# Performance work log

Hardware: AMD Instinct MI355X
Metric: run time of the kernel (lower is better)

Reference implementation:

```python
import jax, jax.numpy as jnp
import numpy as np

L, E, H, D, F, B, CIN, N = 12, 128, 4, 32, 512, 64, 256, 257


def setup_inputs() -> dict:
    key = jax.random.key(0)
    ks = jax.random.split(key, 10)
    s = 0.02
    rn = lambda k, shape: jax.random.normal(k, shape, jnp.float32) * s
    return {
        "feat": jax.random.normal(ks[0], (B, CIN, 32, 32), jnp.float32),
        "conv_w": rn(ks[1], (E, CIN, 3, 3)),
        "conv_b": jnp.zeros((E,), jnp.float32),
        "pos_emb": rn(ks[2], (1, N, E)),
        "cls_token": rn(ks[3], (1, 1, E)),
        "ln1_s": jnp.ones((L, E), jnp.float32),
        "ln1_b": jnp.zeros((L, E), jnp.float32),
        "qkv_w": rn(ks[4], (L, 3 * E, E)),
        "qkv_b": jnp.zeros((L, 3 * E), jnp.float32),
        "proj_w": rn(ks[5], (L, E, E)),
        "proj_b": jnp.zeros((L, E), jnp.float32),
        "ln2_s": jnp.ones((L, E), jnp.float32),
        "ln2_b": jnp.zeros((L, E), jnp.float32),
        "ffn1_w": rn(ks[6], (L, F, E)),
        "ffn1_b": jnp.zeros((L, F), jnp.float32),
        "ffn2_w": rn(ks[7], (L, E, F)),
        "ffn2_b": jnp.zeros((L, E), jnp.float32),
        "fn_s": jnp.ones((E,), jnp.float32),
        "fn_b": jnp.zeros((E,), jnp.float32),
        "fc_w": rn(ks[8], (2, E)),
        "fc_b": jnp.zeros((2,), jnp.float32),
    }


def _ln(x, s, b, eps):
    m = jnp.mean(x, -1, keepdims=True)
    v = jnp.mean((x - m) ** 2, -1, keepdims=True)
    return (x - m) * jax.lax.rsqrt(v + eps) * s + b


def reference(feat, conv_w, conv_b, pos_emb, cls_token, ln1_s, ln1_b, qkv_w,
              qkv_b, proj_w, proj_b, ln2_s, ln2_b, ffn1_w, ffn1_b, ffn2_w,
              ffn2_b, fn_s, fn_b, fc_w, fc_b):
    # patch embed: 3x3 conv stride 2 -> 16x16 = 256 tokens
    emb = jax.lax.conv_general_dilated(
        feat, conv_w, (2, 2), ((1, 1), (1, 1)),
        dimension_numbers=("NCHW", "OIHW", "NCHW")) + conv_b[None, :, None, None]
    Bsz = emb.shape[0]
    emb = emb.reshape(Bsz, E, -1).transpose(0, 2, 1)  # [B, 256, E]
    x = jnp.concatenate([jnp.broadcast_to(cls_token, (Bsz, 1, E)), emb], axis=1)
    x = x + pos_emb  # [B, N, E]
    scale = (E // H) ** -0.5

    def block(x, p):
        l1s, l1b, qw, qb, pw, pb, l2s, l2b, w1, b1, w2, b2 = p
        h = _ln(x, l1s, l1b, 1e-5)
        qkv = (h @ qw.T + qb).reshape(Bsz, N, 3, H, D).transpose(2, 0, 3, 1, 4)
        q, k, v = qkv[0], qkv[1], qkv[2]  # [B, H, N, D]
        att = jax.nn.softmax(jnp.einsum("bhnd,bhmd->bhnm", q, k) * scale, axis=-1)
        o = jnp.einsum("bhnm,bhmd->bhnd", att, v).transpose(0, 2, 1, 3).reshape(Bsz, N, E)
        x = x + (o @ pw.T + pb)
        h2 = _ln(x, l2s, l2b, 1e-5)
        x = x + (jax.nn.gelu(h2 @ w1.T + b1, approximate=False) @ w2.T + b2)
        return x, None

    x, _ = jax.lax.scan(block, x, (ln1_s, ln1_b, qkv_w, qkv_b, proj_w, proj_b,
                                   ln2_s, ln2_b, ffn1_w, ffn1_b, ffn2_w, ffn2_b))
    x = _ln(x, fn_s, fn_b, 1e-6)
    out_feat = x[:, 0, :]
    out = out_feat @ fc_w.T + fc_b
    return (out, out_feat)
```

## Files before the change

### kernel.cpp

```cpp
#include <hip/hip_runtime.h>
#include <math.h>

constexpr int NP_ = 272;
constexpr int MP_ = 64 * NP_;
constexpr int TPB_ = 17;

typedef short short8 __attribute__((ext_vector_type(8)));
typedef float f32x4 __attribute__((ext_vector_type(4)));

__device__ inline short f2bs(float f) {
    unsigned u = __builtin_bit_cast(unsigned, f);
    unsigned r = (u + 0x7fffu + ((u >> 16) & 1u)) >> 16;
    return (short)r;
}

__device__ inline f32x4 mfma16(short8 a, short8 b, f32x4 c) {
    return __builtin_amdgcn_mfma_f32_16x16x32_bf16(a, b, c, 0, 0, 0);
}

__global__ void repack_all(const float* __restrict__ qkvw, const float* __restrict__ projw,
                           const float* __restrict__ f1w, const float* __restrict__ f2w,
                           const float* __restrict__ convw,
                           short* __restrict__ wq, short* __restrict__ wp,
                           short* __restrict__ w1, short* __restrict__ w2,
                           short* __restrict__ wc) {
    int o = blockIdx.x * 256 + threadIdx.x;
    if (o < 589824) {
        int l = o / 49152, r = o % 49152;
        int chunk = r / 3072, w = r % 3072;
        int n = w >> 3, k = chunk * 8 + (w & 7);
        wq[o] = f2bs(qkvw[(size_t)l * 49152 + n * 128 + k]);
        return;
    }
    o -= 589824;
    if (o < 196608) {
        int l = o / 16384, r = o % 16384;
        int chunk = r / 1024, w = r % 1024;
        int n = w >> 3, k = chunk * 8 + (w & 7);
        wp[o] = f2bs(projw[(size_t)l * 16384 + n * 128 + k]);
        return;
    }
    o -= 196608;
    if (o < 786432) {
        int l = o / 65536, r = o % 65536;
        int chunk = r / 4096, w = r % 4096;
        int n = w >> 3, k = chunk * 8 + (w & 7);
        w1[o] = f2bs(f1w[(size_t)l * 65536 + n * 128 + k]);
        return;
    }
    o -= 786432;
    if (o < 786432) {
        int l = o / 65536, r = o % 65536;
        int chunk = r / 1024, w = r % 1024;
        int n = w >> 3, k = chunk * 8 + (w & 7);
        w2[o] = f2bs(f2w[(size_t)l * 65536 + n * 512 + k]);
        return;
    }
    o -= 786432;
    if (o < 294912) {
        int j = o & 7;
        int col = (o >> 3) & 127;
        int c = o >> 10;
        int qd = c & 3, cscb = c >> 2;
        int cs = cscb & 7, kykx = cscb >> 3;
        int cin = cs * 32 + qd * 8 + j;
        int ky = kykx / 3, kx = kykx % 3;
        wc[o] = f2bs(convw[((col * 256 + cin) * 3 + ky) * 3 + kx]);
    }
}

__global__ __launch_bounds__(256) void conv_gemm(const float* __restrict__ feat, const short* __restrict__ wr,
                                                 const float* __restrict__ cb, const float* __restrict__ pos,
                                                 const float* __restrict__ cls, float* __restrict__ X) {
    __shared__ __align__(16) short Ain[3 * 34 * 256];
    int b = blockIdx.x >> 4, oy = blockIdx.x & 15;
    int tid = threadIdx.x;
    for (int idx = tid; idx < 6144; idx += 256) {
        int x4 = idx & 7;
        int cin = (idx >> 3) & 255;
        int r = idx >> 11;
        int y = 2 * oy + r - 1;
        float4 f = make_float4(0.f, 0.f, 0.f, 0.f);
        if (y >= 0 && y < 32)
            f = *(const float4*)(feat + (((size_t)(b * 256 + cin) * 32 + y) * 32 + x4 * 4));
        int cg = cin >> 3, c7 = cin & 7;
        float vv[4] = {f.x, f.y, f.z, f.w};
#pragma unroll
        for (int dx = 0; dx < 4; ++dx) {
            int px = x4 * 4 + 1 + dx;
            int sw = (px >> 1) & 7;
            Ain[(r * 34 + px) * 256 + ((cg ^ sw) * 8) + c7] = f2bs(vv[dx]);
        }
    }
    for (int idx = tid; idx < 1536; idx += 256) {
        int c = idx & 255;
        int j = idx >> 8;
        int r = j >> 1;
        int px = (j & 1) ? 33 : 0;
        Ain[(r * 34 + px) * 256 + c] = 0;
    }
    __syncthreads();
    int wave = tid >> 6, lane = tid & 63;
    int ng = wave, lo = lane & 15, qd = lane >> 4;
    f32x4 acc[2] = {};
#pragma unroll
    for (int ky = 0; ky < 3; ++ky)
#pragma unroll
        for (int kx = 0; kx < 3; ++kx) {
            int sx = 2 * lo + kx;
            int arow = (ky * 34 + sx) * 256;
            int sw = (sx >> 1) & 7;
            const short* wb = wr + (((size_t)((ky * 3 + kx) * 8) * 4 + qd) * 128 + ng * 32 + lo) * 8;
#pragma unroll
            for (int cs = 0; cs < 8; ++cs) {
                short8 af = *(const short8*)(Ain + arow + (((cs * 4 + qd) ^ sw) * 8));
                short8 b0 = *(const short8*)(wb + (size_t)cs * 4096);
                short8 b1 = *(const short8*)(wb + (size_t)cs * 4096 + 128);
                acc[0] = mfma16(af, b0, acc[0]);
                acc[1] = mfma16(af, b1, acc[1]);
            }
        }
#pragma unroll
    for (int t = 0; t < 2; ++t) {
        int e = ng * 32 + t * 16 + lo;
        float bias = cb[e];
#pragma unroll
        for (int r = 0; r < 4; ++r) {
            int tok = 1 + oy * 16 + qd * 4 + r;
            X[((size_t)b * NP_ + tok) * 128 + e] = acc[t][r] + bias + pos[tok * 128 + e];
        }
    }
    if (oy == 0) {
        if (tid < 128) X[(size_t)b * NP_ * 128 + tid] = cls[tid] + pos[tid];
        for (int idx = tid; idx < 15 * 128; idx += 256)
            X[((size_t)b * NP_ + 257) * 128 + idx] = 0.f;
    }
}

__device__ inline void ln_tile16(const float* Xl, const float* __restrict__ s, const float* __restrict__ bb,
                                 short* SB, int tid, float eps) {
    int wv = tid >> 6, lane = tid & 63;
    int r4 = lane & 3, c32 = lane >> 2;
    int row = wv * 4 + r4;
    const float* xr = Xl + row * 132 + c32 * 8;
    float4 a = *(const float4*)(xr);
    float4 b = *(const float4*)(xr + 4);
    float v[8] = {a.x, a.y, a.z, a.w, b.x, b.y, b.z, b.w};
    float sum = v[0] + v[1] + v[2] + v[3] + v[4] + v[5] + v[6] + v[7];
    sum += __shfl_xor(sum, 4); sum += __shfl_xor(sum, 8);
    sum += __shfl_xor(sum, 16); sum += __shfl_xor(sum, 32);
    float mean = sum * (1.f / 128.f);
    float vs = 0.f;
#pragma unroll
    for (int j = 0; j < 8; ++j) { float d = v[j] - mean; vs += d * d; }
    vs += __shfl_xor(vs, 4); vs += __shfl_xor(vs, 8);
    vs += __shfl_xor(vs, 16); vs += __shfl_xor(vs, 32);
    float rs = rsqrtf(vs * (1.f / 128.f) + eps);
    float4 s0 = *(const float4*)(s + c32 * 8), s1 = *(const float4*)(s + c32 * 8 + 4);
    float4 b0 = *(const float4*)(bb + c32 * 8), b1 = *(const float4*)(bb + c32 * 8 + 4);
    float sv[8] = {s0.x, s0.y, s0.z, s0.w, s1.x, s1.y, s1.z, s1.w};
    float bv[8] = {b0.x, b0.y, b0.z, b0.w, b1.x, b1.y, b1.z, b1.w};
    short8 o;
#pragma unroll
    for (int j = 0; j < 8; ++j) o[j] = f2bs((v[j] - mean) * rs * sv[j] + bv[j]);
    *(short8*)(SB + (c32 * 16 + row) * 8) = o;
}

__device__ inline void qkv_stage32(const short* SB, const short* __restrict__ wq, const float* __restrict__ qb,
                                   const short8* pre, int mg, int wv, int lo, int qd,
                                   short* __restrict__ Qf, short* __restrict__ Kf, short* __restrict__ Vt) {
    int n0 = wv * 96;
    f32x4 acc[2][6] = {};
#pragma unroll
    for (int ki = 0; ki < 4; ++ki) {
        int kq = ki * 4 + qd;
        short8 a0 = *(const short8*)(SB + (kq * 16 + lo) * 8);
        short8 a1 = *(const short8*)(SB + 2048 + (kq * 16 + lo) * 8);
#pragma unroll
        for (int t = 0; t < 6; ++t) {
            short8 bf = (ki == 0) ? pre[t]
                                  : *(const short8*)(wq + ((size_t)kq * 384 + n0 + t * 16 + lo) * 8);
            acc[0][t] = mfma16(a0, bf, acc[0][t]);
            acc[1][t] = mfma16(a1, bf, acc[1][t]);
        }
    }
#pragma unroll
    for (int mt = 0; mt < 2; ++mt)
#pragma unroll
        for (int t = 0; t < 6; ++t) {
            int n = n0 + t * 16 + lo;
            float bvv = qb[n];
            int seg = n >> 7, m = n & 127, h = m >> 5, d = m & 31;
#pragma unroll
            for (int r = 0; r < 4; ++r) {
                int row = mg * 32 + mt * 16 + qd * 4 + r;
                int bb2 = row / NP_, q = row - bb2 * NP_;
                short val = f2bs(acc[mt][t][r] + bvv);
                if (seg == 2)
                    Vt[((size_t)(bb2 * 4 + h) * 32 + d) * NP_ + q] = val;
                else
                    (seg ? Kf : Qf)[((size_t)(bb2 * 4 + h) * 4 + (d >> 3)) * (NP_ * 8) + q * 8 + (d & 7)] = val;
            }
        }
}

__global__ __launch_bounds__(256, 3) void qkv0(const float* __restrict__ X, const short* __restrict__ wq,
                                               const float* __restrict__ qb, const float* __restrict__ ls,
                                               const float* __restrict__ lb,
                                               short* __restrict__ Qf, short* __restrict__ Kf,
                                               short* __restrict__ Vt) {
    __shared__ __align__(16) float Xl[32 * 132];
    __shared__ __align__(16) short SB[2 * 2048];
    int mg = blockIdx.x, tid = threadIdx.x;
    int wv = tid >> 6, lane = tid & 63, lo = lane & 15, qd = lane >> 4;
    for (int idx = tid; idx < 1024; idx += 256) {
        int tok = idx >> 5, c = idx & 31;
        *(float4*)(Xl + tok * 132 + c * 4) = *(const float4*)(X + (size_t)(mg * 32 + tok) * 128 + c * 4);
    }
    short8 preq[6];
#pragma unroll
    for (int t = 0; t < 6; ++t)
        preq[t] = *(const short8*)(wq + ((size_t)qd * 384 + wv * 96 + t * 16 + lo) * 8);
    __syncthreads();
    ln_tile16(Xl, ls, lb, SB, tid, 1e-5f);
    ln_tile16(Xl + 16 * 132, ls, lb, SB + 2048, tid, 1e-5f);
    __syncthreads();
    qkv_stage32(SB, wq, qb, preq, mg, wv, lo, qd, Qf, Kf, Vt);
}

template <int LAST>
__global__ __launch_bounds__(256, 3) void layer_tail(
    const short* __restrict__ Of, const short* __restrict__ wp, const float* __restrict__ pb,
    const float* __restrict__ l2s, const float* __restrict__ l2b,
    const short* __restrict__ w1, const float* __restrict__ b1,
    const short* __restrict__ w2, const float* __restrict__ b2,
    float* __restrict__ X,
    const float* __restrict__ l1s, const float* __restrict__ l1b,
    const short* __restrict__ wq, const float* __restrict__ qb,
    short* __restrict__ Qf, short* __restrict__ Kf, short* __restrict__ Vt) {
    __shared__ __align__(16) short SB[2 * 2048];
    __shared__ __align__(16) float Xl[32 * 132];
    __shared__ __align__(16) short Uh[2 * 32 * 136];
    int mg = blockIdx.x, tid = threadIdx.x;
    int wv = tid >> 6, lane = tid & 63, lo = lane & 15, qd = lane >> 4;
    const short* osrc = Of + (size_t)mg * 4096;
    for (int idx = tid; idx < 512; idx += 256)
        *(short8*)(SB + idx * 8) = *(const short8*)(osrc + idx * 8);
    for (int idx = tid; idx < 1024; idx += 256) {
        int tok = idx >> 5, c = idx & 31;
        *(float4*)(Xl + tok * 132 + c * 4) = *(const float4*)(X + (size_t)(mg * 32 + tok) * 128 + c * 4);
    }
    int n0 = wv * 32;
    short8 prep[8];
#pragma unroll
    for (int ki = 0; ki < 4; ++ki) {
        int kq = ki * 4 + qd;
        prep[ki * 2] = *(const short8*)(wp + ((size_t)kq * 128 + n0 + lo) * 8);
        prep[ki * 2 + 1] = *(const short8*)(wp + ((size_t)kq * 128 + n0 + 16 + lo) * 8);
    }
    __syncthreads();
    {
        f32x4 pa[2][2] = {};
#pragma unroll
        for (int ki = 0; ki < 4; ++ki) {
            int kq = ki * 4 + qd;
            short8 a0 = *(const short8*)(SB + (kq * 16 + lo) * 8);
            short8 a1 = *(const short8*)(SB + 2048 + (kq * 16 + lo) * 8);
            pa[0][0] = mfma16(a0, prep[ki * 2], pa[0][0]);
            pa[0][1] = mfma16(a0, prep[ki * 2 + 1], pa[0][1]);
            pa[1][0] = mfma16(a1, prep[ki * 2], pa[1][0]);
            pa[1][1] = mfma16(a1, prep[ki * 2 + 1], pa[1][1]);
        }
        float pb0 = pb[n0 + lo], pb1 = pb[n0 + 16 + lo];
#pragma unroll
        for (int mt = 0; mt < 2; ++mt)
#pragma unroll
            for (int r = 0; r < 4; ++r) {
                Xl[(mt * 16 + qd * 4 + r) * 132 + n0 + lo] += pa[mt][0][r] + pb0;
                Xl[(mt * 16 + qd * 4 + r) * 132 + n0 + 16 + lo] += pa[mt][1][r] + pb1;
            }
    }
    int n0h = wv * 64;
    short8 pre1[4];
#pragma unroll
    for (int t = 0; t < 4; ++t)
        pre1[t] = *(const short8*)(w1 + ((size_t)qd * 512 + n0h + t * 16 + lo) * 8);
    __syncthreads();
    ln_tile16(Xl, l2s, l2b, SB, tid, 1e-5f);
    ln_tile16(Xl + 16 * 132, l2s, l2b, SB + 2048, tid, 1e-5f);
    __syncthreads();
    f32x4 facc[2][2] = {};
    {
        f32x4 fa[2][4] = {};
#pragma unroll
        for (int ki = 0; ki < 4; ++ki) {
            int kq = ki * 4 + qd;
            short8 a0 = *(const short8*)(SB + (kq * 16 + lo) * 8);
            short8 a1 = *(const short8*)(SB + 2048 + (kq * 16 + lo) * 8);
#pragma unroll
            for (int t = 0; t < 4; ++t) {
                short8 bf = (ki == 0) ? pre1[t]
                                      : *(const short8*)(w1 + ((size_t)kq * 512 + n0h + t * 16 + lo) * 8);
                fa[0][t] = mfma16(a0, bf, fa[0][t]);
                fa[1][t] = mfma16(a1, bf, fa[1][t]);
            }
        }
#pragma unroll
        for (int t = 0; t < 4; ++t) {
            int nl = n0h + t * 16 + lo;
            float bvv = b1[nl];
#pragma unroll
            for (int mt = 0; mt < 2; ++mt)
#pragma unroll
                for (int r = 0; r < 4; ++r) {
                    float x = fa[mt][t][r] + bvv;
                    float u = x * (0.7978845608f + 0.0356774081f * x * x);
                    x = x / (1.f + __expf(-2.f * u));
                    Uh[(mt * 32 + (nl >> 3)) * 136 + (qd * 4 + r) * 8 + (nl & 7)] = f2bs(x);
                }
        }
    }
    short8 pre2a = *(const short8*)(w2 + ((size_t)qd * 128 + n0 + lo) * 8);
    short8 pre2b = *(const short8*)(w2 + ((size_t)qd * 128 + n0 + 16 + lo) * 8);
    short8 pre1b[4];
#pragma unroll
    for (int t = 0; t < 4; ++t)
        pre1b[t] = *(const short8*)(w1 + ((size_t)qd * 512 + 256 + n0h + t * 16 + lo) * 8);
    __syncthreads();
#pragma unroll
    for (int ki = 0; ki < 8; ++ki) {
        int kq2 = ki * 4 + qd;
        short8 a0 = *(const short8*)(Uh + kq2 * 136 + lo * 8);
        short8 a1 = *(const short8*)(Uh + (32 + kq2) * 136 + lo * 8);
        short8 b0 = (ki == 0) ? pre2a : *(const short8*)(w2 + ((size_t)kq2 * 128 + n0 + lo) * 8);
        short8 b1 = (ki == 0) ? pre2b : *(const short8*)(w2 + ((size_t)kq2 * 128 + n0 + 16 + lo) * 8);
        facc[0][0] = mfma16(a0, b0, facc[0][0]);
        facc[0][1] = mfma16(a0, b1, facc[0][1]);
        facc[1][0] = mfma16(a1, b0, facc[1][0]);
        facc[1][1] = mfma16(a1, b1, facc[1][1]);
    }
    short8 pre3a = *(const short8*)(w2 + ((size_t)(32 + qd) * 128 + n0 + lo) * 8);
    short8 pre3b = *(const short8*)(w2 + ((size_t)(32 + qd) * 128 + n0 + 16 + lo) * 8);
    __syncthreads();
    {
        f32x4 fa[2][4] = {};
#pragma unroll
        for (int ki = 0; ki < 4; ++ki) {
            int kq = ki * 4 + qd;
            short8 a0 = *(const short8*)(SB + (kq * 16 + lo) * 8);
            short8 a1 = *(const short8*)(SB + 2048 + (kq * 16 + lo) * 8);
#pragma unroll
            for (int t = 0; t < 4; ++t) {
                short8 bf = (ki == 0) ? pre1b[t]
                                      : *(const short8*)(w1 + ((size_t)kq * 512 + 256 + n0h + t * 16 + lo) * 8);
                fa[0][t] = mfma16(a0, bf, fa[0][t]);
                fa[1][t] = mfma16(a1, bf, fa[1][t]);
            }
        }
#pragma unroll
        for (int t = 0; t < 4; ++t) {
            int nl = n0h + t * 16 + lo;
            float bvv = b1[256 + nl];
#pragma unroll
            for (int mt = 0; mt < 2; ++mt)
#pragma unroll
                for (int r = 0; r < 4; ++r) {
                    float x = fa[mt][t][r] + bvv;
                    float u = x * (0.7978845608f + 0.0356774081f * x * x);
                    x = x / (1.f + __expf(-2.f * u));
                    Uh[(mt * 32 + (nl >> 3)) * 136 + (qd * 4 + r) * 8 + (nl & 7)] = f2bs(x);
                }
        }
    }
    __syncthreads();
#pragma unroll
    for (int ki = 0; ki < 8; ++ki) {
        int kq2 = ki * 4 + qd;
        short8 a0 = *(const short8*)(Uh + kq2 * 136 + lo * 8);
        short8 a1 = *(const short8*)(Uh + (32 + kq2) * 136 + lo * 8);
        short8 b0 = (ki == 0) ? pre3a : *(const short8*)(w2 + ((size_t)(32 + kq2) * 128 + n0 + lo) * 8);
        short8 b1 = (ki == 0) ? pre3b : *(const short8*)(w2 + ((size_t)(32 + kq2) * 128 + n0 + 16 + lo) * 8);
        facc[0][0] = mfma16(a0, b0, facc[0][0]);
        facc[0][1] = mfma16(a0, b1, facc[0][1]);
        facc[1][0] = mfma16(a1, b0, facc[1][0]);
        facc[1][1] = mfma16(a1, b1, facc[1][1]);
    }
    {
        float b20 = b2[n0 + lo], b21 = b2[n0 + 16 + lo];
#pragma unroll
        for (int mt = 0; mt < 2; ++mt)
#pragma unroll
            for (int r = 0; r < 4; ++r) {
                Xl[(mt * 16 + qd * 4 + r) * 132 + n0 + lo] += facc[mt][0][r] + b20;
                Xl[(mt * 16 + qd * 4 + r) * 132 + n0 + 16 + lo] += facc[mt][1][r] + b21;
            }
    }
    short8 preq[6];
    if (!LAST) {
#pragma unroll
        for (int t = 0; t < 6; ++t)
            preq[t] = *(const short8*)(wq + ((size_t)qd * 384 + wv * 96 + t * 16 + lo) * 8);
    }
    __syncthreads();
    for (int idx = tid; idx < 1024; idx += 256) {
        int tok = idx >> 5, c = idx & 31;
        *(float4*)(X + (size_t)(mg * 32 + tok) * 128 + c * 4) = *(const float4*)(Xl + tok * 132 + c * 4);
    }
    if (LAST) return;
    ln_tile16(Xl, l1s, l1b, SB, tid, 1e-5f);
    ln_tile16(Xl + 16 * 132, l1s, l1b, SB + 2048, tid, 1e-5f);
    __syncthreads();
    qkv_stage32(SB, wq, qb, preq, mg, wv, lo, qd, Qf, Kf, Vt);
}

__global__ __launch_bounds__(256, 4) void attn(const short* __restrict__ Qf, const short* __restrict__ Kf,
                                               const short* __restrict__ Vt, short* __restrict__ Of) {
    __shared__ __align__(16) short Vl[32 * 296];
    __shared__ __align__(16) short Pl[4][544];
    int b = blockIdx.x >> 4, h = (blockIdx.x >> 2) & 3, qc = blockIdx.x & 3;
    int tid = threadIdx.x;
    const short* kf = Kf + (size_t)(b * 4 + h) * (4 * NP_ * 8);
    const short* qf = Qf + (size_t)(b * 4 + h) * (4 * NP_ * 8);
    const short* vt = Vt + (size_t)(b * 4 + h) * (32 * NP_);
    for (int idx = tid; idx < 32 * 37; idx += 256) {
        int d = idx / 37, c8 = idx - d * 37;
        short8 v = {};
        if (c8 < 34) v = *(const short8*)(vt + d * NP_ + c8 * 8);
        *(short8*)(Vl + d * 296 + c8 * 8) = v;
    }
    __syncthreads();
    int wv = tid >> 6, lane = tid & 63, lo = lane & 15, qd = lane >> 4;
    short* Pw = Pl[wv];
    const float scale = 0.17677669529663687f;
    for (int it = 0; it < 2; ++it) {
        int qt;
        if (it == 0) qt = qc * 4 + wv;
        else { if ((qc | wv) != 0) break; qt = 16; }
        short8 qfr = *(const short8*)(qf + ((size_t)qd * NP_ + qt * 16 + lo) * 8);
        f32x4 sc[17];
#pragma unroll
        for (int kt = 0; kt < 17; ++kt) {
            short8 kfr = *(const short8*)(kf + ((size_t)qd * NP_ + kt * 16 + lo) * 8);
            f32x4 z = {};
            sc[kt] = mfma16(qfr, kfr, z);
        }
        float mx[4] = {-1e30f, -1e30f, -1e30f, -1e30f};
#pragma unroll
        for (int kt = 0; kt < 17; ++kt) {
            bool valid = (kt * 16 + lo) < 257;
#pragma unroll
            for (int r = 0; r < 4; ++r) {
                float v2 = valid ? sc[kt][r] * scale : -1e30f;
                sc[kt][r] = v2;
                mx[r] = fmaxf(mx[r], v2);
            }
        }
#pragma unroll
        for (int r = 0; r < 4; ++r) {
            mx[r] = fmaxf(mx[r], __shfl_xor(mx[r], 1));
            mx[r] = fmaxf(mx[r], __shfl_xor(mx[r], 2));
            mx[r] = fmaxf(mx[r], __shfl_xor(mx[r], 4));
            mx[r] = fmaxf(mx[r], __shfl_xor(mx[r], 8));
        }
        float l[4] = {0.f, 0.f, 0.f, 0.f};
#pragma unroll
        for (int kt = 0; kt < 17; ++kt)
#pragma unroll
            for (int r = 0; r < 4; ++r) {
                float p = __expf(sc[kt][r] - mx[r]);
                sc[kt][r] = p;
                l[r] += p;
            }
#pragma unroll
        for (int r = 0; r < 4; ++r) {
            l[r] += __shfl_xor(l[r], 1);
            l[r] += __shfl_xor(l[r], 2);
            l[r] += __shfl_xor(l[r], 4);
            l[r] += __shfl_xor(l[r], 8);
        }
        float rl[4];
#pragma unroll
        for (int r = 0; r < 4; ++r) rl[r] = 1.f / l[r];
        f32x4 oa[2] = {};
#pragma unroll
        for (int ks = 0; ks < 9; ++ks) {
#pragma unroll
            for (int kt2 = 0; kt2 < 2; ++kt2) {
                int kt = ks * 2 + kt2;
                int lkey = kt2 * 16 + lo;
#pragma unroll
                for (int r = 0; r < 4; ++r) {
                    short pv = (kt < 17) ? f2bs(sc[kt][r] * rl[r]) : (short)0;
                    Pw[(lkey >> 3) * 128 + (qd * 4 + r) * 8 + (lkey & 7)] = pv;
                }
            }
            short8 pf = *(const short8*)(Pw + (qd * 16 + lo) * 8);
#pragma unroll
            for (int nt = 0; nt < 2; ++nt) {
                short8 vfr = *(const short8*)(Vl + (nt * 16 + lo) * 296 + ks * 32 + qd * 8);
                oa[nt] = mfma16(pf, vfr, oa[nt]);
            }
        }
        int tile = b * TPB_ + qt;
#pragma unroll
        for (int nt = 0; nt < 2; ++nt)
#pragma unroll
            for (int r = 0; r < 4; ++r) {
                int qq = qt * 16 + qd * 4 + r;
                if (qq <= 256) {
                    int col = h * 32 + nt * 16 + lo;
                    Of[(size_t)tile * 2048 + (col >> 3) * 128 + (qd * 4 + r) * 8 + (col & 7)] = f2bs(oa[nt][r]);
                }
            }
    }
}

__global__ __launch_bounds__(64) void final_head(const float* __restrict__ X, const float* __restrict__ fs,
                                                 const float* __restrict__ fb, const float* __restrict__ fcw,
                                                 const float* __restrict__ fcb, float* __restrict__ out) {
    int b = blockIdx.x, lane = threadIdx.x;
    float2 v = *(const float2*)(X + (size_t)b * NP_ * 128 + lane * 2);
    float sum = v.x + v.y;
#pragma unroll
    for (int m = 1; m < 64; m <<= 1) sum += __shfl_xor(sum, m);
    float mean = sum * (1.f / 128.f);
    float d0 = v.x - mean, d1 = v.y - mean;
    float vs = d0 * d0 + d1 * d1;
#pragma unroll
    for (int m = 1; m < 64; m <<= 1) vs += __shfl_xor(vs, m);
    float rs = rsqrtf(vs * (1.f / 128.f) + 1e-6f);
    int e = lane * 2;
    float f0 = d0 * rs * fs[e] + fb[e];
    float f1 = d1 * rs * fs[e + 1] + fb[e + 1];
    out[128 + b * 128 + e] = f0;
    out[128 + b * 128 + e + 1] = f1;
    float p0 = f0 * fcw[e] + f1 * fcw[e + 1];
    float p1 = f0 * fcw[128 + e] + f1 * fcw[128 + e + 1];
#pragma unroll
    for (int m = 1; m < 64; m <<= 1) {
        p0 += __shfl_xor(p0, m);
        p1 += __shfl_xor(p1, m);
    }
    if (lane == 0) {
        out[b * 2 + 0] = p0 + fcb[0];
        out[b * 2 + 1] = p1 + fcb[1];
    }
}

extern "C" void kernel_launch(void* const* d_in, const int* in_sizes, int n_in,
                              void* d_out, int out_size, void* d_ws, size_t ws_size,
                              hipStream_t stream) {
    const float* feat    = (const float*)d_in[0];
    const float* conv_w  = (const float*)d_in[1];
    const float* conv_b  = (const float*)d_in[2];
    const float* pos_emb = (const float*)d_in[3];
    const float* cls_tok = (const float*)d_in[4];
    const float* ln1_s   = (const float*)d_in[5];
    const float* ln1_b   = (const float*)d_in[6];
    const float* qkv_w   = (const float*)d_in[7];
    const float* qkv_b   = (const float*)d_in[8];
    const float* proj_w  = (const float*)d_in[9];
    const float* proj_b  = (const float*)d_in[10];
    const float* ln2_s   = (const float*)d_in[11];
    const float* ln2_b   = (const float*)d_in[12];
    const float* ffn1_w  = (const float*)d_in[13];
    const float* ffn1_b  = (const float*)d_in[14];
    const float* ffn2_w  = (const float*)d_in[15];
    const float* ffn2_b  = (const float*)d_in[16];
    const float* fn_s    = (const float*)d_in[17];
    const float* fn_b    = (const float*)d_in[18];
    const float* fc_w    = (const float*)d_in[19];
    const float* fc_b    = (const float*)d_in[20];

    char* p = (char*)d_ws;
    auto alloc = [&](size_t bytes) { char* r = p; p += (bytes + 255) & ~(size_t)255; return r; };
    short* wq  = (short*)alloc((size_t)589824 * 2);
    short* wp  = (short*)alloc((size_t)196608 * 2);
    short* w1  = (short*)alloc((size_t)786432 * 2);
    short* w2  = (short*)alloc((size_t)786432 * 2);
    short* wc  = (short*)alloc((size_t)294912 * 2);
    float* X   = (float*)alloc((size_t)MP_ * 128 * 4);
    short* Qf  = (short*)alloc((size_t)64 * 16 * NP_ * 8 * 2);
    short* Kf  = (short*)alloc((size_t)64 * 16 * NP_ * 8 * 2);
    short* Vt  = (short*)alloc((size_t)64 * 4 * 32 * NP_ * 2);
    short* Of  = (short*)alloc((size_t)(MP_ / 16) * 2048 * 2);

    repack_all<<<10368, 256, 0, stream>>>(qkv_w, proj_w, ffn1_w, ffn2_w, conv_w, wq, wp, w1, w2, wc);
    conv_gemm<<<1024, 256, 0, stream>>>(feat, wc, conv_b, pos_emb, cls_tok, X);

    qkv0<<<544, 256, 0, stream>>>(X, wq, qkv_b, ln1_s, ln1_b, Qf, Kf, Vt);
    for (int l = 0; l < 12; ++l) {
        attn<<<1024, 256, 0, stream>>>(Qf, Kf, Vt, Of);
        if (l < 11)
            layer_tail<0><<<544, 256, 0, stream>>>(Of, wp + (size_t)l * 16384, proj_b + l * 128,
                                                   ln2_s + l * 128, ln2_b + l * 128,
                                                   w1 + (size_t)l * 65536, ffn1_b + l * 512,
                                                   w2 + (size_t)l * 65536, ffn2_b + l * 128, X,
                                                   ln1_s + (l + 1) * 128, ln1_b + (l + 1) * 128,
                                                   wq + (size_t)(l + 1) * 49152, qkv_b + (l + 1) * 384,
                                                   Qf, Kf, Vt);
        else
            layer_tail<1><<<544, 256, 0, stream>>>(Of, wp + (size_t)l * 16384, proj_b + l * 128,
                                                   ln2_s + l * 128, ln2_b + l * 128,
                                                   w1 + (size_t)l * 65536, ffn1_b + l * 512,
                                                   w2 + (size_t)l * 65536, ffn2_b + l * 128, X,
                                                   ln1_s, ln1_b, wq, qkv_b, Qf, Kf, Vt);
    }
    final_head<<<64, 64, 0, stream>>>(X, fn_s, fn_b, fc_w, fc_b, (float*)d_out);
}
```

Before: 782.2 us.

## Stage conv input through padded LDS transpose, fold softmax scale and normalization

The conv patch-embed kernel now loads the input in 64-channel slices through a padded shared-memory transpose buffer, prefetching the next slice while the current one is packed. Each thread then writes eight channels as a single 16-byte LDS store instead of scattered 2-byte stores. Separately, the attention scale is folded into Q at the QKV epilogue and softmax normalization is deferred to the output. V writes and LayerNorm packing are vectorized with a paired bf16 conversion. The conv loop adds two barriers per slice, and Q is now rounded to bf16 after scaling, which slightly changes rounding.

```diff
diff --git a/kernel.cpp b/kernel.cpp
--- a/kernel.cpp
+++ b/kernel.cpp
@@ -12,6 +12,14 @@
     unsigned u = __builtin_bit_cast(unsigned, f);
     unsigned r = (u + 0x7fffu + ((u >> 16) & 1u)) >> 16;
     return (short)r;
+}
+
+__device__ inline unsigned f2bs2(float a, float b) {
+    unsigned ua = __builtin_bit_cast(unsigned, a);
+    unsigned ub = __builtin_bit_cast(unsigned, b);
+    unsigned ra = (ua + 0x7fffu + ((ua >> 16) & 1u)) >> 16;
+    unsigned rb = (ub + 0x7fffu + ((ub >> 16) & 1u)) & 0xffff0000u;
+    return ra | rb;
 }
 
 __device__ inline f32x4 mfma16(short8 a, short8 b, f32x4 c) {
@@ -73,25 +81,9 @@
                                                  const float* __restrict__ cb, const float* __restrict__ pos,
                                                  const float* __restrict__ cls, float* __restrict__ X) {
     __shared__ __align__(16) short Ain[3 * 34 * 256];
+    __shared__ float tmp[64 * 33];
     int b = blockIdx.x >> 4, oy = blockIdx.x & 15;
     int tid = threadIdx.x;
-    for (int idx = tid; idx < 6144; idx += 256) {
-        int x4 = idx & 7;
-        int cin = (idx >> 3) & 255;
-        int r = idx >> 11;
-        int y = 2 * oy + r - 1;
-        float4 f = make_float4(0.f, 0.f, 0.f, 0.f);
-        if (y >= 0 && y < 32)
-            f = *(const float4*)(feat + (((size_t)(b * 256 + cin) * 32 + y) * 32 + x4 * 4));
-        int cg = cin >> 3, c7 = cin & 7;
-        float vv[4] = {f.x, f.y, f.z, f.w};
-#pragma unroll
-        for (int dx = 0; dx < 4; ++dx) {
-            int px = x4 * 4 + 1 + dx;
-            int sw = (px >> 1) & 7;
-            Ain[(r * 34 + px) * 256 + ((cg ^ sw) * 8) + c7] = f2bs(vv[dx]);
-        }
-    }
     for (int idx = tid; idx < 1536; idx += 256) {
         int c = idx & 255;
         int j = idx >> 8;
@@ -99,7 +91,57 @@
         int px = (j & 1) ? 33 : 0;
         Ain[(r * 34 + px) * 256 + c] = 0;
     }
-    __syncthreads();
+    auto load_slice = [&](int s, float4& A, float4& B) {
+        int r = s >> 2, cbase = (s & 3) * 64;
+        int y = 2 * oy + r - 1;
+        A = make_float4(0.f, 0.f, 0.f, 0.f);
+        B = A;
+        if (y >= 0 && y < 32) {
+            int cl = tid >> 3, x4 = tid & 7;
+            A = *(const float4*)(feat + (((size_t)(b * 256 + cbase + cl) * 32 + y) * 32 + x4 * 4));
+            int i2 = tid + 256;
+            int cl2 = i2 >> 3, x42 = i2 & 7;
+            B = *(const float4*)(feat + (((size_t)(b * 256 + cbase + cl2) * 32 + y) * 32 + x42 * 4));
+        }
+    };
+    float4 ra, rb;
+    load_slice(0, ra, rb);
+    for (int s = 0; s < 12; ++s) {
+        int rr = s >> 2, cbase = (s & 3) * 64;
+        {
+            int cl = tid >> 3, x4 = tid & 7;
+            tmp[cl * 33 + x4 * 4 + 0] = ra.x;
+            tmp[cl * 33 + x4 * 4 + 1] = ra.y;
+            tmp[cl * 33 + x4 * 4 + 2] = ra.z;
+            tmp[cl * 33 + x4 * 4 + 3] = ra.w;
+            int i2 = tid + 256;
+            int cl2 = i2 >> 3, x42 = i2 & 7;
+            tmp[cl2 * 33 + x42 * 4 + 0] = rb.x;
+            tmp[cl2 * 33 + x42 * 4 + 1] = rb.y;
+            tmp[cl2 * 33 + x42 * 4 + 2] = rb.z;
+            tmp[cl2 * 33 + x42 * 4 + 3] = rb.w;
+        }
+        __syncthreads();
+        float4 na, nb;
+        if (s < 11) load_slice(s + 1, na, nb);
+        {
+            int px = 1 + (tid & 31), g = tid >> 5;
+            int sw = (px >> 1) & 7;
+            int cg = (cbase >> 3) + g;
+            float f[8];
+#pragma unroll
+            for (int j = 0; j < 8; ++j) f[j] = tmp[(g * 8 + j) * 33 + (px - 1)];
+            uint4 ov;
+            ov.x = f2bs2(f[0], f[1]);
+            ov.y = f2bs2(f[2], f[3]);
+            ov.z = f2bs2(f[4], f[5]);
+            ov.w = f2bs2(f[6], f[7]);
+            *(uint4*)(Ain + (rr * 34 + px) * 256 + ((cg ^ sw) * 8)) = ov;
+        }
+        __syncthreads();
+        ra = na;
+        rb = nb;
+    }
     int wave = tid >> 6, lane = tid & 63;
     int ng = wave, lo = lane & 15, qd = lane >> 4;
     f32x4 acc[2] = {};
@@ -160,10 +202,15 @@
     float4 b0 = *(const float4*)(bb + c32 * 8), b1 = *(const float4*)(bb + c32 * 8 + 4);
     float sv[8] = {s0.x, s0.y, s0.z, s0.w, s1.x, s1.y, s1.z, s1.w};
     float bv[8] = {b0.x, b0.y, b0.z, b0.w, b1.x, b1.y, b1.z, b1.w};
-    short8 o;
-#pragma unroll
-    for (int j = 0; j < 8; ++j) o[j] = f2bs((v[j] - mean) * rs * sv[j] + bv[j]);
-    *(short8*)(SB + (c32 * 16 + row) * 8) = o;
+    float y[8];
+#pragma unroll
+    for (int j = 0; j < 8; ++j) y[j] = (v[j] - mean) * rs * sv[j] + bv[j];
+    uint4 ov;
+    ov.x = f2bs2(y[0], y[1]);
+    ov.y = f2bs2(y[2], y[3]);
+    ov.z = f2bs2(y[4], y[5]);
+    ov.w = f2bs2(y[6], y[7]);
+    *(uint4*)(SB + (c32 * 16 + row) * 8) = ov;
 }
 
 __device__ inline void qkv_stage32(const short* SB, const short* __restrict__ wq, const float* __restrict__ qb,
@@ -191,15 +238,20 @@
             int n = n0 + t * 16 + lo;
             float bvv = qb[n];
             int seg = n >> 7, m = n & 127, h = m >> 5, d = m & 31;
-#pragma unroll
-            for (int r = 0; r < 4; ++r) {
-                int row = mg * 32 + mt * 16 + qd * 4 + r;
-                int bb2 = row / NP_, q = row - bb2 * NP_;
-                short val = f2bs(acc[mt][t][r] + bvv);
-                if (seg == 2)
-                    Vt[((size_t)(bb2 * 4 + h) * 32 + d) * NP_ + q] = val;
-                else
-                    (seg ? Kf : Qf)[((size_t)(bb2 * 4 + h) * 4 + (d >> 3)) * (NP_ * 8) + q * 8 + (d & 7)] = val;
+            int row0 = mg * 32 + mt * 16 + qd * 4;
+            int bb2 = row0 / NP_, q0 = row0 - bb2 * NP_;
+            if (seg == 2) {
+                uint2 u;
+                u.x = f2bs2(acc[mt][t][0] + bvv, acc[mt][t][1] + bvv);
+                u.y = f2bs2(acc[mt][t][2] + bvv, acc[mt][t][3] + bvv);
+                *(uint2*)(Vt + ((size_t)(bb2 * 4 + h) * 32 + d) * NP_ + q0) = u;
+            } else {
+                float qs = (seg == 0) ? 0.17677669529663687f : 1.f;
+#pragma unroll
+                for (int r = 0; r < 4; ++r) {
+                    short val = f2bs((acc[mt][t][r] + bvv) * qs);
+                    (seg ? Kf : Qf)[((size_t)(bb2 * 4 + h) * 4 + (d >> 3)) * (NP_ * 8) + (q0 + r) * 8 + (d & 7)] = val;
+                }
             }
         }
 }
@@ -431,7 +483,6 @@
     __syncthreads();
     int wv = tid >> 6, lane = tid & 63, lo = lane & 15, qd = lane >> 4;
     short* Pw = Pl[wv];
-    const float scale = 0.17677669529663687f;
     for (int it = 0; it < 2; ++it) {
         int qt;
         if (it == 0) qt = qc * 4 + wv;
@@ -450,7 +501,7 @@
             bool valid = (kt * 16 + lo) < 257;
 #pragma unroll
             for (int r = 0; r < 4; ++r) {
-                float v2 = valid ? sc[kt][r] * scale : -1e30f;
+                float v2 = valid ? sc[kt][r] : -1e30f;
                 sc[kt][r] = v2;
                 mx[r] = fmaxf(mx[r], v2);
             }
@@ -490,7 +541,7 @@
                 int lkey = kt2 * 16 + lo;
 #pragma unroll
                 for (int r = 0; r < 4; ++r) {
-                    short pv = (kt < 17) ? f2bs(sc[kt][r] * rl[r]) : (short)0;
+                    short pv = (kt < 17) ? f2bs(sc[kt][r]) : (short)0;
                     Pw[(lkey >> 3) * 128 + (qd * 4 + r) * 8 + (lkey & 7)] = pv;
                 }
             }
@@ -509,7 +560,7 @@
                 int qq = qt * 16 + qd * 4 + r;
                 if (qq <= 256) {
                     int col = h * 32 + nt * 16 + lo;
-                    Of[(size_t)tile * 2048 + (col >> 3) * 128 + (qd * 4 + r) * 8 + (col & 7)] = f2bs(oa[nt][r]);
+                    Of[(size_t)tile * 2048 + (col >> 3) * 128 + (qd * 4 + r) * 8 + (col & 7)] = f2bs(oa[nt][r] * rl[r]);
                 }
             }
     }
```

New measurement: 717.3 us. 8.3% less time.
